# Kernel optimization log

Measured on AMD Instinct MI355X. Metric: run time of the kernel, lower is better.

Reference implementation:

```python
import jax, jax.numpy as jnp
import numpy as np

B, T, E = 4, 2048, 1024
H, D = 16, 64  # n_heads, head_size


def setup_inputs() -> dict:
    key = jax.random.key(0)
    ks = jax.random.split(key, 6)
    s = 0.02
    x = jax.random.normal(ks[0], (B, T, E), dtype=jnp.float32)
    Wq = jax.random.normal(ks[1], (H, E, D), dtype=jnp.float32) * s
    Wk = jax.random.normal(ks[2], (H, E, D), dtype=jnp.float32) * s
    Wv = jax.random.normal(ks[3], (H, E, D), dtype=jnp.float32) * s
    Wp = jax.random.normal(ks[4], (E, E), dtype=jnp.float32) * s
    bp = jnp.zeros((E,), dtype=jnp.float32)
    return {"x": x, "Wq": Wq, "Wk": Wk, "Wv": Wv, "Wp": Wp, "bp": bp}


def reference(x, Wq, Wk, Wv, Wp, bp):
    # Per-head bias-free Q/K/V projections (vectorized over heads)
    q = jnp.einsum('bte,hed->bhtd', x, Wq)
    k = jnp.einsum('bte,hed->bhtd', x, Wk)
    v = jnp.einsum('bte,hed->bhtd', x, Wv)
    scale = 1.0 / jnp.sqrt(jnp.asarray(D, dtype=x.dtype))
    scores = jnp.einsum('bhtd,bhsd->bhts', q, k) * scale  # [B,H,T,T]
    causal = jnp.tril(jnp.ones((T, T), dtype=bool))
    scores = jnp.where(causal, scores, jnp.asarray(-jnp.inf, dtype=scores.dtype))
    attn = jax.nn.softmax(scores, axis=-1)
    out = jnp.einsum('bhts,bhsd->bhtd', attn, v)  # [B,H,T,D]
    # concat heads: 'nh b t c -> b t (nh c)'
    out = out.transpose(0, 2, 1, 3).reshape(B, T, H * D)
    # output projection (dropout p=0.0 is identity)
    return out @ Wp.T + bp
```

## Files before the change

kernel.cpp:

```cpp
#include <hip/hip_runtime.h>

typedef unsigned short u16;
typedef __attribute__((ext_vector_type(8))) short bf16x8;
typedef __attribute__((ext_vector_type(4))) short bf16x4;
typedef __attribute__((ext_vector_type(4))) float f32x4;

__device__ __forceinline__ u16 f2bf(float f) {
  unsigned u = __float_as_uint(f);
  u += 0x7FFFu + ((u >> 16) & 1u);
  return (u16)(u >> 16);
}
__device__ __forceinline__ unsigned pack2(float a, float b) {
  return (unsigned)f2bf(a) | ((unsigned)f2bf(b) << 16);
}
#if __has_builtin(__builtin_amdgcn_cvt_pk_bf16_f32)
typedef __attribute__((ext_vector_type(2))) __bf16 bf16v2;
__device__ __forceinline__ unsigned cvt_pk(float a, float b) {
  bf16v2 v = __builtin_amdgcn_cvt_pk_bf16_f32(a, b);
  return __builtin_bit_cast(unsigned, v);
}
#else
__device__ __forceinline__ unsigned cvt_pk(float a, float b) { return pack2(a, b); }
#endif
__device__ __forceinline__ uint4 pack8(float4 a, float4 b) {
  uint4 r;
  r.x = pack2(a.x, a.y); r.y = pack2(a.z, a.w);
  r.z = pack2(b.x, b.y); r.w = pack2(b.z, b.w);
  return r;
}
__device__ __forceinline__ void gload16(const void* g, void* l) {
  __builtin_amdgcn_global_load_lds(
      (const __attribute__((address_space(1))) void*)g,
      (__attribute__((address_space(3))) void*)l, 16, 0, 0);
}
__device__ __forceinline__ f32x4 mfma16(bf16x4 a, bf16x4 b, f32x4 c) {
#if __has_builtin(__builtin_amdgcn_mfma_f32_16x16x16bf16_1k)
  return __builtin_amdgcn_mfma_f32_16x16x16bf16_1k(a, b, c, 0, 0, 0);
#elif __has_builtin(__builtin_amdgcn_mfma_f32_16x16x16_bf16)
  return __builtin_amdgcn_mfma_f32_16x16x16_bf16(a, b, c, 0, 0, 0);
#else
  asm volatile("v_mfma_f32_16x16x16_bf16 %0, %1, %2, %0\n\ts_nop 2"
               : "+v"(c) : "v"(a), "v"(b));
  return c;
#endif
}

__global__ __launch_bounds__(256) void prep(
    const float* __restrict__ x, u16* __restrict__ xbf,
    const float* __restrict__ Wq, const float* __restrict__ Wk,
    const float* __restrict__ Wv, u16* __restrict__ wt,
    const float* __restrict__ Wp, u16* __restrict__ wpbf) {
  const int tid = threadIdx.x;
  const int b = blockIdx.x;
  __shared__ __align__(16) u16 tile[64 * 72];
  if (b < 4096) {
    const size_t i = (size_t)b * 256 + tid;
    const float4* p = (const float4*)(x + i * 8);
    *(uint4*)(xbf + i * 8) = pack8(p[0], p[1]);
  } else if (b < 4864) {
    const int idx = b - 4096;
    const int w = idx >> 8;
    const int mat = (idx >> 4) & 15;
    const int r0 = (idx & 15) * 64;
    const float* src = (w == 0 ? Wq : (w == 1 ? Wk : Wv)) + (size_t)mat * 1024 * 64;
    u16* dst = wt + (size_t)w * 1024 * 1024 + (size_t)mat * 1024 * 64;
#pragma unroll
    for (int i = 0; i < 2; ++i) {
      const int c = tid + i * 256;
      const int r = c >> 3, off = (c & 7) * 8;
      const float* p = src + (size_t)(r0 + r) * 64 + off;
      *(uint4*)(&tile[r * 72 + off]) = pack8(*(const float4*)p, *(const float4*)(p + 4));
    }
    __syncthreads();
#pragma unroll
    for (int i = 0; i < 2; ++i) {
      const int c = tid + i * 256;
      const int d = c >> 3, roff = (c & 7) * 8;
      bf16x8 v;
#pragma unroll
      for (int j = 0; j < 8; ++j) v[j] = (short)tile[(roff + j) * 72 + d];
      *(bf16x8*)(dst + (size_t)d * 1024 + r0 + roff) = v;
    }
  } else {
    const size_t i = (size_t)(b - 4864) * 256 + tid;
    const float4* p = (const float4*)(Wp + i * 8);
    *(uint4*)(wpbf + i * 8) = pack8(p[0], p[1]);
  }
}

template <int MODE>
__global__ __launch_bounds__(256) void gemm_bt(
    const u16* __restrict__ A, const u16* __restrict__ BT,
    u16* __restrict__ o0, u16* __restrict__ o1, u16* __restrict__ o2,
    float* __restrict__ fout, const float* __restrict__ bp) {
  __shared__ __align__(16) u16 As[128 * 32];
  __shared__ __align__(16) u16 Bs[128 * 32];
  const int tid = threadIdx.x;
  const int lane = tid & 63, wv = tid >> 6;
  const int g = lane >> 4, ln = lane & 15;
  const int wm = wv >> 1, wn = wv & 1;
  const int m0 = blockIdx.x * 128, n0 = blockIdx.y * 128;

  const f32x4 fz = {0.f, 0.f, 0.f, 0.f};
  f32x4 acc[4][4];
#pragma unroll
  for (int i = 0; i < 4; ++i)
#pragma unroll
    for (int j = 0; j < 4; ++j) acc[i][j] = fz;

  for (int k0 = 0; k0 < 1024; k0 += 32) {
    __syncthreads();
#pragma unroll
    for (int i = 0; i < 2; ++i) {
      const int c = tid + i * 256;
      const int r = c >> 2, off = (c & 3) * 8;
      gload16(A + (size_t)(m0 + r) * 1024 + k0 + off, &As[c * 8]);
      gload16(BT + (size_t)(n0 + r) * 1024 + k0 + off, &Bs[c * 8]);
    }
    __syncthreads();
    bf16x8 af[4], bfr[4];
#pragma unroll
    for (int rt = 0; rt < 4; ++rt)
      af[rt] = *(const bf16x8*)(&As[(wm * 64 + rt * 16 + ln) * 32 + g * 8]);
#pragma unroll
    for (int ct = 0; ct < 4; ++ct)
      bfr[ct] = *(const bf16x8*)(&Bs[(wn * 64 + ct * 16 + ln) * 32 + g * 8]);
#pragma unroll
    for (int rt = 0; rt < 4; ++rt)
#pragma unroll
      for (int ct = 0; ct < 4; ++ct)
        acc[rt][ct] = __builtin_amdgcn_mfma_f32_16x16x32_bf16(af[rt], bfr[ct],
                                                              acc[rt][ct], 0, 0, 0);
  }

  if (MODE == 0) {
    const int which = n0 >> 10;
    const int nl0 = (n0 & 1023) + wn * 64;
    const float qs = (which == 0) ? 0.1803368801f : 1.0f;
    if (which < 2) {
      u16* outp = which == 0 ? o0 : o1;
#pragma unroll
      for (int rt = 0; rt < 4; ++rt)
#pragma unroll
        for (int ct = 0; ct < 4; ++ct) {
          const int nl = nl0 + ct * 16 + ln;
          const int h = nl >> 6, d = nl & 63;
#pragma unroll
          for (int r = 0; r < 4; ++r) {
            const int m = m0 + wm * 64 + rt * 16 + 4 * g + r;
            const int b = m >> 11, t = m & 2047;
            outp[(((size_t)(b * 16 + h) * 2048 + t) << 6) + d] =
                f2bf(acc[rt][ct][r] * qs);
          }
        }
    } else {
#pragma unroll
      for (int rt = 0; rt < 4; ++rt) {
        const int tb = m0 + wm * 64 + rt * 16 + 4 * g;
        const int b = tb >> 11, t = tb & 2047;
#pragma unroll
        for (int ct = 0; ct < 4; ++ct) {
          const int nl = nl0 + ct * 16 + ln;
          const int h = nl >> 6, d = nl & 63;
          u16* dst = o2 + ((size_t)((b * 16 + h) * 64 + d) << 11) + t;
#pragma unroll
          for (int r = 0; r < 4; ++r) dst[r] = f2bf(acc[rt][ct][r]);
        }
      }
    }
  } else {
#pragma unroll
    for (int ct = 0; ct < 4; ++ct) {
      const int n = n0 + wn * 64 + ct * 16 + ln;
      const float bias = bp[n];
#pragma unroll
      for (int rt = 0; rt < 4; ++rt)
#pragma unroll
        for (int r = 0; r < 4; ++r) {
          const int m = m0 + wm * 64 + rt * 16 + 4 * g + r;
          fout[(size_t)m * 1024 + n] = acc[rt][ct][r] + bias;
        }
    }
  }
}

__global__ __launch_bounds__(256) void attn_kernel(
    const u16* __restrict__ Q, const u16* __restrict__ K,
    const u16* __restrict__ VT, u16* __restrict__ AO) {
  const int tid = threadIdx.x;
  const int wv = tid >> 6, lane = tid & 63, g = lane >> 4, ln = lane & 15;
  const int bh = blockIdx.x;
  const int jb = blockIdx.y;
  const u16* Qb = Q + (size_t)bh * (2048 * 64);
  const u16* Kb = K + (size_t)bh * (2048 * 64);
  const u16* Vb = VT + (size_t)bh * (64 * 2048);

  __shared__ __align__(16) u16 Ks[64 * 72];
  __shared__ __align__(16) u16 Vs[64 * 72];

  const int sr0 = tid >> 3, so0 = (tid & 7) * 8;
  const int sr1 = sr0 + 32;

  uint4 kpf0 = *(const uint4*)(Kb + (size_t)sr0 * 64 + so0);
  uint4 kpf1 = *(const uint4*)(Kb + (size_t)sr1 * 64 + so0);
  uint4 vpf0 = *(const uint4*)(Vb + (size_t)sr0 * 2048 + so0);
  uint4 vpf1 = *(const uint4*)(Vb + (size_t)sr1 * 2048 + so0);

  const int b = bh >> 4, h = bh & 15;
  const short ob = 0x3F80;
  const bf16x4 ones = {ob, ob, ob, ob};
  const f32x4 fz = {0.f, 0.f, 0.f, 0.f};

#pragma unroll
  for (int ph = 0; ph < 2; ++ph) {
    const int qi = (ph == 0) ? jb : 15 - jb;
    const int q0 = qi * 128;
    const int nt = 2 * qi + 2;
    const int ntw = 2 * qi + 1 + (wv >> 1);

    bf16x8 qa[2][2];
#pragma unroll
    for (int rt = 0; rt < 2; ++rt) {
      const int row = q0 + wv * 32 + rt * 16 + ln;
#pragma unroll
      for (int hh = 0; hh < 2; ++hh)
        qa[rt][hh] = *(const bf16x8*)(Qb + (size_t)row * 64 + hh * 32 + g * 8);
    }

    f32x4 oacc[2][4], lacc[2];
#pragma unroll
    for (int rt = 0; rt < 2; ++rt) {
      lacc[rt] = fz;
#pragma unroll
      for (int dt = 0; dt < 4; ++dt) oacc[rt][dt] = fz;
    }

    for (int kt = 0; kt < nt; ++kt) {
      __syncthreads();
      *(uint4*)(&Ks[sr0 * 72 + so0]) = kpf0;
      *(uint4*)(&Ks[sr1 * 72 + so0]) = kpf1;
      *(uint4*)(&Vs[sr0 * 72 + so0]) = vpf0;
      *(uint4*)(&Vs[sr1 * 72 + so0]) = vpf1;
      __syncthreads();
      if ((kt + 1 < nt) || (ph == 0)) {
        const int sn = (kt + 1 < nt) ? (kt + 1) * 64 : 0;
        kpf0 = *(const uint4*)(Kb + (size_t)(sn + sr0) * 64 + so0);
        kpf1 = *(const uint4*)(Kb + (size_t)(sn + sr1) * 64 + so0);
        vpf0 = *(const uint4*)(Vb + (size_t)sr0 * 2048 + sn + so0);
        vpf1 = *(const uint4*)(Vb + (size_t)sr1 * 2048 + sn + so0);
      }
      if (kt < ntw) {
        const int s0 = kt * 64;
        f32x4 sfT[2][4];
#pragma unroll
        for (int rt = 0; rt < 2; ++rt)
#pragma unroll
          for (int st = 0; st < 4; ++st) sfT[rt][st] = fz;
#pragma unroll
        for (int st = 0; st < 4; ++st) {
          const bf16x8 kb0 = *(const bf16x8*)(&Ks[(st * 16 + ln) * 72 + g * 8]);
          const bf16x8 kb1 = *(const bf16x8*)(&Ks[(st * 16 + ln) * 72 + 32 + g * 8]);
#pragma unroll
          for (int rt = 0; rt < 2; ++rt) {
            sfT[rt][st] = __builtin_amdgcn_mfma_f32_16x16x32_bf16(kb0, qa[rt][0],
                                                                  sfT[rt][st], 0, 0, 0);
            sfT[rt][st] = __builtin_amdgcn_mfma_f32_16x16x32_bf16(kb1, qa[rt][1],
                                                                  sfT[rt][st], 0, 0, 0);
          }
        }
        const bool diag = (kt == ntw - 1);
        bf16x4 pa[2][4];
#pragma unroll
        for (int rt = 0; rt < 2; ++rt) {
          const int qloc = wv * 32 + rt * 16 + ln;
#pragma unroll
          for (int st = 0; st < 4; ++st) {
            float e[4];
#pragma unroll
            for (int r = 0; r < 4; ++r) e[r] = __builtin_amdgcn_exp2f(sfT[rt][st][r]);
            if (diag) {
              const int sloc = s0 - q0 + st * 16 + 4 * g;
#pragma unroll
              for (int r = 0; r < 4; ++r)
                if (sloc + r > qloc) e[r] = 0.f;
            }
            uint2 packed = {cvt_pk(e[0], e[1]), cvt_pk(e[2], e[3])};
            pa[rt][st] = __builtin_bit_cast(bf16x4, packed);
          }
        }
#pragma unroll
        for (int st = 0; st < 4; ++st) {
#pragma unroll
          for (int dt = 0; dt < 4; ++dt) {
            const bf16x4 vb =
                *(const bf16x4*)(&Vs[(dt * 16 + ln) * 72 + st * 16 + 4 * g]);
#pragma unroll
            for (int rt = 0; rt < 2; ++rt)
              oacc[rt][dt] = mfma16(pa[rt][st], vb, oacc[rt][dt]);
          }
#pragma unroll
          for (int rt = 0; rt < 2; ++rt)
            lacc[rt] = mfma16(pa[rt][st], ones, lacc[rt]);
        }
      }
    }
#pragma unroll
    for (int rt = 0; rt < 2; ++rt) {
      float linv[4];
#pragma unroll
      for (int r = 0; r < 4; ++r) linv[r] = 1.f / lacc[rt][r];
#pragma unroll
      for (int dt = 0; dt < 4; ++dt)
#pragma unroll
        for (int r = 0; r < 4; ++r) {
          const int qg = q0 + wv * 32 + rt * 16 + 4 * g + r;
          AO[(size_t)(b * 2048 + qg) * 1024 + h * 64 + dt * 16 + ln] =
              f2bf(oacc[rt][dt][r] * linv[r]);
        }
    }
  }
}

extern "C" void kernel_launch(void* const* d_in, const int* in_sizes, int n_in,
                              void* d_out, int out_size, void* d_ws, size_t ws_size,
                              hipStream_t stream) {
  const float* x  = (const float*)d_in[0];
  const float* Wq = (const float*)d_in[1];
  const float* Wk = (const float*)d_in[2];
  const float* Wv = (const float*)d_in[3];
  const float* Wp = (const float*)d_in[4];
  const float* bp = (const float*)d_in[5];
  float* out = (float*)d_out;

  char* ws = (char*)d_ws;
  const size_t MB = 1048576;
  u16* xbf  = (u16*)(ws);
  u16* aows = (u16*)(ws);
  u16* wt   = (u16*)(ws + 16 * MB);
  u16* wpbf = (u16*)(ws + 22 * MB);
  u16* qws  = (u16*)(ws + 24 * MB);
  u16* kws  = (u16*)(ws + 40 * MB);
  u16* vtws = (u16*)(ws + 56 * MB);

  prep<<<dim3(5376), 256, 0, stream>>>(x, xbf, Wq, Wk, Wv, wt, Wp, wpbf);
  gemm_bt<0><<<dim3(64, 24), 256, 0, stream>>>(xbf, wt, qws, kws, vtws,
                                               nullptr, nullptr);
  attn_kernel<<<dim3(64, 8), 256, 0, stream>>>(qws, kws, vtws, aows);
  gemm_bt<1><<<dim3(64, 8), 256, 0, stream>>>(aows, wpbf, nullptr, nullptr,
                                              nullptr, out, bp);
}
```

Before: 268.2 us.

## Deepen GEMM K-step to 64, use hardware bf16 pack, vectorize V-transpose stores

The projection GEMM now loads a 64-wide K slab per iteration into two 32-wide LDS halves, which halves the number of barrier pairs per tile. The software round-to-nearest bf16 conversions in the epilogues and in the fp32-to-bf16 pack helper are replaced with the hardware packed conversion when it is available. The transposed V epilogue writes four bf16 values as one 8-byte store. In the attention kernel, score accumulators are no longer zeroed explicitly; the first MFMA takes a zero input instead. LDS use in the GEMM doubles, which may reduce occupancy.

```diff
diff --git a/kernel.cpp b/kernel.cpp
--- a/kernel.cpp
+++ b/kernel.cpp
@@ -24,8 +24,8 @@
 #endif
 __device__ __forceinline__ uint4 pack8(float4 a, float4 b) {
   uint4 r;
-  r.x = pack2(a.x, a.y); r.y = pack2(a.z, a.w);
-  r.z = pack2(b.x, b.y); r.w = pack2(b.z, b.w);
+  r.x = cvt_pk(a.x, a.y); r.y = cvt_pk(a.z, a.w);
+  r.z = cvt_pk(b.x, b.y); r.w = cvt_pk(b.z, b.w);
   return r;
 }
 __device__ __forceinline__ void gload16(const void* g, void* l) {
@@ -93,8 +93,8 @@
     const u16* __restrict__ A, const u16* __restrict__ BT,
     u16* __restrict__ o0, u16* __restrict__ o1, u16* __restrict__ o2,
     float* __restrict__ fout, const float* __restrict__ bp) {
-  __shared__ __align__(16) u16 As[128 * 32];
-  __shared__ __align__(16) u16 Bs[128 * 32];
+  __shared__ __align__(16) u16 As[2][128 * 32];
+  __shared__ __align__(16) u16 Bs[2][128 * 32];
   const int tid = threadIdx.x;
   const int lane = tid & 63, wv = tid >> 6;
   const int g = lane >> 4, ln = lane & 15;
@@ -108,29 +108,34 @@
 #pragma unroll
     for (int j = 0; j < 4; ++j) acc[i][j] = fz;
 
-  for (int k0 = 0; k0 < 1024; k0 += 32) {
+  for (int k0 = 0; k0 < 1024; k0 += 64) {
     __syncthreads();
 #pragma unroll
-    for (int i = 0; i < 2; ++i) {
-      const int c = tid + i * 256;
-      const int r = c >> 2, off = (c & 3) * 8;
-      gload16(A + (size_t)(m0 + r) * 1024 + k0 + off, &As[c * 8]);
-      gload16(BT + (size_t)(n0 + r) * 1024 + k0 + off, &Bs[c * 8]);
-    }
+    for (int hf = 0; hf < 2; ++hf)
+#pragma unroll
+      for (int j = 0; j < 2; ++j) {
+        const int c = j * 256 + tid;
+        const int r = c >> 2, off = (c & 3) * 8;
+        gload16(A + (size_t)(m0 + r) * 1024 + k0 + hf * 32 + off, &As[hf][c * 8]);
+        gload16(BT + (size_t)(n0 + r) * 1024 + k0 + hf * 32 + off, &Bs[hf][c * 8]);
+      }
     __syncthreads();
-    bf16x8 af[4], bfr[4];
-#pragma unroll
-    for (int rt = 0; rt < 4; ++rt)
-      af[rt] = *(const bf16x8*)(&As[(wm * 64 + rt * 16 + ln) * 32 + g * 8]);
-#pragma unroll
-    for (int ct = 0; ct < 4; ++ct)
-      bfr[ct] = *(const bf16x8*)(&Bs[(wn * 64 + ct * 16 + ln) * 32 + g * 8]);
-#pragma unroll
-    for (int rt = 0; rt < 4; ++rt)
+#pragma unroll
+    for (int hf = 0; hf < 2; ++hf) {
+      bf16x8 af[4], bfr[4];
+#pragma unroll
+      for (int rt = 0; rt < 4; ++rt)
+        af[rt] = *(const bf16x8*)(&As[hf][(wm * 64 + rt * 16 + ln) * 32 + g * 8]);
 #pragma unroll
       for (int ct = 0; ct < 4; ++ct)
-        acc[rt][ct] = __builtin_amdgcn_mfma_f32_16x16x32_bf16(af[rt], bfr[ct],
-                                                              acc[rt][ct], 0, 0, 0);
+        bfr[ct] = *(const bf16x8*)(&Bs[hf][(wn * 64 + ct * 16 + ln) * 32 + g * 8]);
+#pragma unroll
+      for (int rt = 0; rt < 4; ++rt)
+#pragma unroll
+        for (int ct = 0; ct < 4; ++ct)
+          acc[rt][ct] = __builtin_amdgcn_mfma_f32_16x16x32_bf16(af[rt], bfr[ct],
+                                                                acc[rt][ct], 0, 0, 0);
+    }
   }
 
   if (MODE == 0) {
@@ -145,12 +150,14 @@
         for (int ct = 0; ct < 4; ++ct) {
           const int nl = nl0 + ct * 16 + ln;
           const int h = nl >> 6, d = nl & 63;
+          const unsigned p01 = cvt_pk(acc[rt][ct][0] * qs, acc[rt][ct][1] * qs);
+          const unsigned p23 = cvt_pk(acc[rt][ct][2] * qs, acc[rt][ct][3] * qs);
+          const u16 vv[4] = {(u16)p01, (u16)(p01 >> 16), (u16)p23, (u16)(p23 >> 16)};
 #pragma unroll
           for (int r = 0; r < 4; ++r) {
             const int m = m0 + wm * 64 + rt * 16 + 4 * g + r;
             const int b = m >> 11, t = m & 2047;
-            outp[(((size_t)(b * 16 + h) * 2048 + t) << 6) + d] =
-                f2bf(acc[rt][ct][r] * qs);
+            outp[(((size_t)(b * 16 + h) * 2048 + t) << 6) + d] = vv[r];
           }
         }
     } else {
@@ -162,9 +169,10 @@
         for (int ct = 0; ct < 4; ++ct) {
           const int nl = nl0 + ct * 16 + ln;
           const int h = nl >> 6, d = nl & 63;
-          u16* dst = o2 + ((size_t)((b * 16 + h) * 64 + d) << 11) + t;
-#pragma unroll
-          for (int r = 0; r < 4; ++r) dst[r] = f2bf(acc[rt][ct][r]);
+          uint2 pv;
+          pv.x = cvt_pk(acc[rt][ct][0], acc[rt][ct][1]);
+          pv.y = cvt_pk(acc[rt][ct][2], acc[rt][ct][3]);
+          *(uint2*)(o2 + ((size_t)((b * 16 + h) * 64 + d) << 11) + t) = pv;
         }
       }
     }
@@ -253,17 +261,13 @@
         const int s0 = kt * 64;
         f32x4 sfT[2][4];
 #pragma unroll
-        for (int rt = 0; rt < 2; ++rt)
-#pragma unroll
-          for (int st = 0; st < 4; ++st) sfT[rt][st] = fz;
-#pragma unroll
         for (int st = 0; st < 4; ++st) {
           const bf16x8 kb0 = *(const bf16x8*)(&Ks[(st * 16 + ln) * 72 + g * 8]);
           const bf16x8 kb1 = *(const bf16x8*)(&Ks[(st * 16 + ln) * 72 + 32 + g * 8]);
 #pragma unroll
           for (int rt = 0; rt < 2; ++rt) {
             sfT[rt][st] = __builtin_amdgcn_mfma_f32_16x16x32_bf16(kb0, qa[rt][0],
-                                                                  sfT[rt][st], 0, 0, 0);
+                                                                  fz, 0, 0, 0);
             sfT[rt][st] = __builtin_amdgcn_mfma_f32_16x16x32_bf16(kb1, qa[rt][1],
                                                                   sfT[rt][st], 0, 0, 0);
           }
@@ -310,13 +314,18 @@
 #pragma unroll
       for (int r = 0; r < 4; ++r) linv[r] = 1.f / lacc[rt][r];
 #pragma unroll
-      for (int dt = 0; dt < 4; ++dt)
+      for (int dt = 0; dt < 4; ++dt) {
+        const unsigned p01 =
+            cvt_pk(oacc[rt][dt][0] * linv[0], oacc[rt][dt][1] * linv[1]);
+        const unsigned p23 =
+            cvt_pk(oacc[rt][dt][2] * linv[2], oacc[rt][dt][3] * linv[3]);
+        const u16 vv[4] = {(u16)p01, (u16)(p01 >> 16), (u16)p23, (u16)(p23 >> 16)};
 #pragma unroll
         for (int r = 0; r < 4; ++r) {
           const int qg = q0 + wv * 32 + rt * 16 + 4 * g + r;
-          AO[(size_t)(b * 2048 + qg) * 1024 + h * 64 + dt * 16 + ln] =
-              f2bf(oacc[rt][dt][r] * linv[r]);
-        }
+          AO[(size_t)(b * 2048 + qg) * 1024 + h * 64 + dt * 16 + ln] = vv[r];
+        }
+      }
     }
   }
 }
```

Result: no change. 263.4 us (-1.8%).
